# Kernel optimization log

Measured on AMD Instinct MI355X. Metric: run time of the kernel, lower is better.

## Reference

```python
import jax, jax.numpy as jnp
import numpy as np

N_NODES = 50000
N_EDGES = 800000
X_DIM = 32
S_DIM = 16
H_DIM = 96   # = 2 * (X_DIM + S_DIM), edge-MLP input
O_DIM = 64


def setup_inputs() -> dict:
    key = jax.random.key(0)
    ks = jax.random.split(key, 6)
    x = jax.random.normal(ks[0], (N_NODES, X_DIM), dtype=jnp.float32)
    scalars = jax.random.normal(ks[1], (1, S_DIM), dtype=jnp.float32)
    W1 = jax.random.normal(ks[2], (H_DIM, H_DIM), dtype=jnp.float32) * (1.0 / np.sqrt(H_DIM))
    b1 = jnp.zeros((H_DIM,), dtype=jnp.float32)
    W2 = jax.random.normal(ks[3], (H_DIM, O_DIM), dtype=jnp.float32) * (1.0 / np.sqrt(H_DIM))
    b2 = jnp.zeros((O_DIM,), dtype=jnp.float32)
    edge_index = jax.random.randint(ks[4], (2, N_EDGES), 0, N_NODES, dtype=jnp.int64)
    return {"x": x, "scalars": scalars, "W1": W1, "b1": b1, "W2": W2,
            "b2": b2, "edge_index": edge_index}


def reference(x, scalars, W1, b1, W2, b2, edge_index):
    n = x.shape[0]
    # single-graph branch of EFN: expand scalars to every node, concat
    s = jnp.broadcast_to(scalars.reshape(1, -1), (n, scalars.shape[-1]))
    h = jnp.concatenate([x, s], axis=1)                      # [N, 48]
    src, dst = edge_index[0], edge_index[1]
    # PTConv: edge-wise MLP on cat([x_i, x_j - x_i]), sum-aggregate to i (dst)
    h_i = h[dst]                                             # [E, 48] gather
    h_j = h[src]                                             # [E, 48] gather
    m_in = jnp.concatenate([h_i, h_j - h_i], axis=1)         # [E, 96]
    m = jax.nn.relu(m_in @ W1 + b1) @ W2 + b2                # [E, 64]
    out = jax.ops.segment_sum(m, dst, num_segments=n)        # [N, 64] scatter-add
    return out
```

## Files before the change

### kernel.cpp

```cpp
#include <hip/hip_runtime.h>


typedef _Float16 half8 __attribute__((ext_vector_type(8)));
typedef _Float16 half4 __attribute__((ext_vector_type(4)));
typedef _Float16 half2t __attribute__((ext_vector_type(2)));
typedef float f32x4 __attribute__((ext_vector_type(4)));
typedef float f32x2 __attribute__((ext_vector_type(2)));

#define LDK 72
#define LDW2 104
#define LDH 104
#define BCAP 1024
#define NBMAX 1563
#define BSTRIDE 16

static __device__ __forceinline__ unsigned char f32_to_fp8(float v) {
    int p = __builtin_amdgcn_cvt_pk_fp8_f32(v, v, 0, false);
    return (unsigned char)(p & 0xff);
}

__global__ __launch_bounds__(512) void prep_kernel(
    const float* __restrict__ x, const float* __restrict__ scalars,
    const float* __restrict__ W1, const float* __restrict__ b1,
    const float* __restrict__ W2, _Float16* __restrict__ W2T,
    _Float16* __restrict__ Pbuf, unsigned char* __restrict__ Qf8,
    const int* __restrict__ src, const int* __restrict__ dst,
    int* __restrict__ bcur, unsigned int* __restrict__ pairs,
    int tiles, int n_e4, int epb4, int nb, int nplace)
{
    __shared__ union {
        struct { int h[NBMAX]; int cur[NBMAX]; } pl;
        _Float16 sW[192 * LDK];
    } sm;
    const int tid = threadIdx.x;

    if ((int)blockIdx.x < nplace) {
        int* h = sm.pl.h;
        int* cur = sm.pl.cur;
        for (int b = tid; b < nb; b += 512) h[b] = 0;
        __syncthreads();

        const int base4 = blockIdx.x * epb4;
        for (int i = tid; i < epb4; i += 512) {
            int i4 = base4 + i;
            if (i4 < n_e4) {
                int4 d = ((const int4*)dst)[i4];
                atomicAdd(&h[d.x >> 5], 1);
                atomicAdd(&h[d.y >> 5], 1);
                atomicAdd(&h[d.z >> 5], 1);
                atomicAdd(&h[d.w >> 5], 1);
            }
        }
        __syncthreads();
        for (int b = tid; b < nb; b += 512) {
            int c = h[b];
            cur[b] = b * BCAP + (c ? atomicAdd(&bcur[b * BSTRIDE], c) : 0);
        }
        __syncthreads();
        for (int i = tid; i < epb4; i += 512) {
            int i4 = base4 + i;
            if (i4 < n_e4) {
                int4 s = ((const int4*)src)[i4];
                int4 d = ((const int4*)dst)[i4];
                int p;
                p = atomicAdd(&cur[d.x >> 5], 1);
                if (p < (d.x >> 5) * BCAP + BCAP) pairs[p] = (unsigned)s.x | ((unsigned)(d.x & 31) << 16);
                p = atomicAdd(&cur[d.y >> 5], 1);
                if (p < (d.y >> 5) * BCAP + BCAP) pairs[p] = (unsigned)s.y | ((unsigned)(d.y & 31) << 16);
                p = atomicAdd(&cur[d.z >> 5], 1);
                if (p < (d.z >> 5) * BCAP + BCAP) pairs[p] = (unsigned)s.z | ((unsigned)(d.z & 31) << 16);
                p = atomicAdd(&cur[d.w >> 5], 1);
                if (p < (d.w >> 5) * BCAP + BCAP) pairs[p] = (unsigned)s.w | ((unsigned)(d.w & 31) << 16);
            }
        }
    } else {
        _Float16* sW = sm.sW;
        for (int idx = tid; idx < 192 * 64; idx += 512) {
            int n = idx >> 6, k = idx & 63;
            float v = 0.f;
            if (k < 48)
                v = (n < 96) ? (W1[k * 96 + n] - W1[(k + 48) * 96 + n])
                             : W1[(k + 48) * 96 + (n - 96)];
            sW[n * LDK + k] = (_Float16)v;
        }
        const int pb = blockIdx.x - nplace;
        if (pb == 0) {
            for (int idx = tid; idx < 96 * 64; idx += 512) {
                int k = idx / 64, n = idx - k * 64;
                W2T[n * 96 + k] = (_Float16)W2[idx];
            }
        }
        __syncthreads();

        const int wave = tid >> 6, lane = tid & 63;
        const int quad = lane >> 4, r = lane & 15;
        const int stride = (gridDim.x - nplace) * 8;

        f32x4 bbv[6];
        #pragma unroll
        for (int nt = 0; nt < 6; ++nt)
            bbv[nt] = *(const f32x4*)&b1[nt * 16 + quad * 4];

        for (int tile = pb * 8 + wave; tile < tiles; tile += stride) {
            const int node = tile * 16 + r;

            half8 a0, a1;
            {
                const f32x4* xp = (const f32x4*)(x + (size_t)node * 32 + quad * 8);
                f32x4 v0 = xp[0], v1 = xp[1];
                #pragma unroll
                for (int j = 0; j < 4; ++j) {
                    a0[j] = (_Float16)v0[j];
                    a0[4 + j] = (_Float16)v1[j];
                }
                #pragma unroll
                for (int j = 0; j < 8; ++j) {
                    int k2 = 32 + quad * 8 + j;
                    a1[j] = (k2 < 48) ? (_Float16)scalars[k2 - 32] : (_Float16)0.f;
                }
            }

            #pragma unroll
            for (int nt = 0; nt < 12; ++nt) {
                f32x4 c = {0.f, 0.f, 0.f, 0.f};
                half8 b0 = *(const half8*)&sW[(nt * 16 + r) * LDK + quad * 8];
                half8 b1v = *(const half8*)&sW[(nt * 16 + r) * LDK + 32 + quad * 8];
                c = __builtin_amdgcn_mfma_f32_16x16x32_f16(b0, a0, c, 0, 0, 0);
                c = __builtin_amdgcn_mfma_f32_16x16x32_f16(b1v, a1, c, 0, 0, 0);
                if (nt < 6) {
                    const int colbase = nt * 16 + quad * 4;
                    half4 pv;
                    #pragma unroll
                    for (int i = 0; i < 4; ++i)
                        pv[i] = (_Float16)(c[i] + bbv[nt][i]);
                    *(half4*)&Pbuf[(size_t)node * 96 + colbase] = pv;
                } else {
                    const int colbase = (nt - 6) * 16 + quad * 4;
                    int lo = __builtin_amdgcn_cvt_pk_fp8_f32(c[0], c[1], 0, false);
                    int full = __builtin_amdgcn_cvt_pk_fp8_f32(c[2], c[3], lo, true);
                    *(unsigned int*)&Qf8[(size_t)node * 96 + colbase] = (unsigned)full;
                }
            }
        }
    }
}

static __device__ __forceinline__ void acc_edge(
    float* __restrict__ ac, const float* __restrict__ pf,
    unsigned int q0, unsigned int q1, unsigned int q2)
{
    f32x2 v;
    v = __builtin_amdgcn_cvt_pk_f32_fp8((int)q0, false);
    { float t0 = pf[0] + v[0], t1 = pf[1] + v[1];
      ac[0] += t0 > 0.f ? t0 : 0.f; ac[1] += t1 > 0.f ? t1 : 0.f; }
    v = __builtin_amdgcn_cvt_pk_f32_fp8((int)q0, true);
    { float t0 = pf[2] + v[0], t1 = pf[3] + v[1];
      ac[2] += t0 > 0.f ? t0 : 0.f; ac[3] += t1 > 0.f ? t1 : 0.f; }
    v = __builtin_amdgcn_cvt_pk_f32_fp8((int)q1, false);
    { float t0 = pf[4] + v[0], t1 = pf[5] + v[1];
      ac[4] += t0 > 0.f ? t0 : 0.f; ac[5] += t1 > 0.f ? t1 : 0.f; }
    v = __builtin_amdgcn_cvt_pk_f32_fp8((int)q1, true);
    { float t0 = pf[6] + v[0], t1 = pf[7] + v[1];
      ac[6] += t0 > 0.f ? t0 : 0.f; ac[7] += t1 > 0.f ? t1 : 0.f; }
    v = __builtin_amdgcn_cvt_pk_f32_fp8((int)q2, false);
    { float t0 = pf[8] + v[0], t1 = pf[9] + v[1];
      ac[8] += t0 > 0.f ? t0 : 0.f; ac[9] += t1 > 0.f ? t1 : 0.f; }
    v = __builtin_amdgcn_cvt_pk_f32_fp8((int)q2, true);
    { float t0 = pf[10] + v[0], t1 = pf[11] + v[1];
      ac[10] += t0 > 0.f ? t0 : 0.f; ac[11] += t1 > 0.f ? t1 : 0.f; }
}

__global__ __launch_bounds__(256) void sgo_kernel(
    const _Float16* __restrict__ Pbuf, const unsigned char* __restrict__ Qf8,
    const int* __restrict__ bcur, const unsigned int* __restrict__ pairs,
    const _Float16* __restrict__ W2T, const float* __restrict__ b2,
    float* __restrict__ out, int n_nodes)
{
    __shared__ unsigned short s_sorted[BCAP];
    __shared__ _Float16 sW2T[64 * LDW2];
    __shared__ _Float16 sH[32 * LDH];
    __shared__ int s_cnt[32];
    __shared__ int s_off[33];
    __shared__ int s_cur[32];

    const int b = blockIdx.x;
    const int tid = threadIdx.x;
    const int lo_g = b * BCAP;
    int cnt = bcur[b * BSTRIDE];
    if (cnt > BCAP) cnt = BCAP;

    half8 w2r[3];
    #pragma unroll
    for (int t = 0; t < 3; ++t) {
        int idx = tid + t * 256;
        int n = idx / 12, c = idx - n * 12;
        w2r[t] = *(const half8*)&W2T[n * 96 + c * 8];
    }

    const int wave = tid >> 6, lane = tid & 63;
    const int g = lane >> 3, j = lane & 7;
    const int ni = wave * 8 + g;
    const int node = b * 32 + ni;

    float pf[12];
    if (node < n_nodes) {
        const unsigned int* Pp = (const unsigned int*)(Pbuf + (size_t)node * 96);
        #pragma unroll
        for (int t = 0; t < 6; ++t) {
            half2t h = __builtin_bit_cast(half2t, Pp[j * 6 + t]);
            pf[2 * t] = (float)h[0];
            pf[2 * t + 1] = (float)h[1];
        }
    }

    unsigned int ureg[4];
    int nit = 0;
    for (int i = tid; i < cnt; i += 256) ureg[nit++] = pairs[lo_g + i];

    if (tid < 32) s_cnt[tid] = 0;
    __syncthreads();

    for (int t = 0; t < nit; ++t)
        atomicAdd(&s_cnt[(ureg[t] >> 16) & 31], 1);
    __syncthreads();
    if (tid == 0) {
        int a = 0;
        #pragma unroll
        for (int l = 0; l < 32; ++l) { s_off[l] = a; a += s_cnt[l]; }
        s_off[32] = a;
    }
    __syncthreads();
    if (tid < 32) s_cur[tid] = s_off[tid];
    __syncthreads();
    for (int t = 0; t < nit; ++t) {
        unsigned int u = ureg[t];
        int p = atomicAdd(&s_cur[(u >> 16) & 31], 1);
        s_sorted[p] = (unsigned short)(u & 0xffffu);
    }
    __syncthreads();

    #pragma unroll
    for (int t = 0; t < 3; ++t) {
        int idx = tid + t * 256;
        int n = idx / 12, c = idx - n * 12;
        *(half8*)&sW2T[n * LDW2 + c * 8] = w2r[t];
    }

    if (node < n_nodes) {
        const int lo = s_off[ni], hi = s_off[ni + 1];

        float ac[12];
        #pragma unroll
        for (int k = 0; k < 12; ++k) ac[k] = 0.f;

        if (lo < hi) {
            const int last = hi - 1;
            unsigned int A0, A1, A2, B0, B1, B2;
            {
                int s0 = s_sorted[lo];
                int i1 = lo + 1 <= last ? lo + 1 : last;
                int s1 = s_sorted[i1];
                const unsigned int* Q0 = (const unsigned int*)(Qf8 + (size_t)s0 * 96) + j * 3;
                const unsigned int* Q1 = (const unsigned int*)(Qf8 + (size_t)s1 * 96) + j * 3;
                A0 = Q0[0]; A1 = Q0[1]; A2 = Q0[2];
                B0 = Q1[0]; B1 = Q1[1]; B2 = Q1[2];
            }
            for (int i = lo; i < hi; i += 2) {
                int i2 = i + 2 <= last ? i + 2 : last;
                int i3 = i + 3 <= last ? i + 3 : last;
                int s2 = s_sorted[i2], s3 = s_sorted[i3];
                const unsigned int* Q2 = (const unsigned int*)(Qf8 + (size_t)s2 * 96) + j * 3;
                const unsigned int* Q3 = (const unsigned int*)(Qf8 + (size_t)s3 * 96) + j * 3;
                unsigned int NA0 = Q2[0], NA1 = Q2[1], NA2 = Q2[2];
                unsigned int NB0 = Q3[0], NB1 = Q3[1], NB2 = Q3[2];
                acc_edge(ac, pf, A0, A1, A2);
                if (i + 1 < hi) acc_edge(ac, pf, B0, B1, B2);
                A0 = NA0; A1 = NA1; A2 = NA2;
                B0 = NB0; B1 = NB1; B2 = NB2;
            }
        }

        unsigned int* Hp = (unsigned int*)sH + ni * (LDH / 2);
        #pragma unroll
        for (int t = 0; t < 6; ++t) {
            half2t hv;
            hv[0] = (_Float16)ac[2 * t];
            hv[1] = (_Float16)ac[2 * t + 1];
            Hp[j * 6 + t] = __builtin_bit_cast(unsigned int, hv);
        }
    }
    __syncthreads();

    const int quad = lane >> 4, r = lane & 15;
    const int t = wave >> 1;
    const int nt0 = (wave & 1) * 2;

    half8 a[3];
    #pragma unroll
    for (int kk = 0; kk < 3; ++kk)
        a[kk] = *(const half8*)&sH[(t * 16 + r) * LDH + kk * 32 + quad * 8];

    #pragma unroll
    for (int w = 0; w < 2; ++w) {
        const int nt = nt0 + w;
        f32x4 c = {0.f, 0.f, 0.f, 0.f};
        #pragma unroll
        for (int kk = 0; kk < 3; ++kk) {
            half8 bfrag = *(const half8*)&sW2T[(nt * 16 + r) * LDW2 + kk * 32 + quad * 8];
            c = __builtin_amdgcn_mfma_f32_16x16x32_f16(a[kk], bfrag, c, 0, 0, 0);
        }
        const int col = nt * 16 + r;
        const float bb = b2[col];
        #pragma unroll
        for (int i = 0; i < 4; ++i) {
            int local = t * 16 + quad * 4 + i;
            int nd = b * 32 + local;
            if (nd < n_nodes) {
                int dg = s_off[local + 1] - s_off[local];
                out[(size_t)nd * 64 + col] = c[i] + dg * bb;
            }
        }
    }
}

extern "C" void kernel_launch(void* const* d_in, const int* in_sizes, int n_in,
                              void* d_out, int out_size, void* d_ws, size_t ws_size,
                              hipStream_t stream) {
    const float* x       = (const float*)d_in[0];
    const float* scalars = (const float*)d_in[1];
    const float* W1      = (const float*)d_in[2];
    const float* b1      = (const float*)d_in[3];
    const float* W2      = (const float*)d_in[4];
    const float* b2      = (const float*)d_in[5];
    const int*   ei      = (const int*)d_in[6];
    float* out = (float*)d_out;

    const int n_edges = in_sizes[6] / 2;
    const int n_nodes = in_sizes[0] / 32;
    const int* src = ei;
    const int* dst = ei + n_edges;
    const int nb = (n_nodes + 31) / 32;
    const int tiles = n_nodes / 16;

    char* w = (char*)d_ws;
    _Float16* Pbuf = (_Float16*)w;          w += (size_t)n_nodes * 96 * 2;
    unsigned char* Qf8 = (unsigned char*)w; w += (size_t)n_nodes * 96;
    unsigned int* pairs = (unsigned int*)w; w += (size_t)nb * BCAP * 4;
    _Float16* W2T = (_Float16*)w;           w += (size_t)96 * 64 * 2;
    int* bcur = (int*)w;                    w += (size_t)nb * BSTRIDE * 4;

    hipMemsetAsync(bcur, 0, (size_t)nb * BSTRIDE * 4, stream);

    const int nplace = 80;
    const int n_e4 = n_edges / 4;
    const int epb4 = (n_e4 + nplace - 1) / nplace;
    prep_kernel<<<dim3(256), dim3(512), 0, stream>>>(
        x, scalars, W1, b1, W2, W2T, Pbuf, Qf8, src, dst, bcur, pairs,
        tiles, n_e4, epb4, nb, nplace);

    sgo_kernel<<<dim3(nb), dim3(256), 0, stream>>>(
        Pbuf, Qf8, bcur, pairs, W2T, b2, out, n_nodes);
}
```

Before: 122.0 us.

## Balance edge work across node groups with contiguous edge ranges and LDS atomics

Result: slower. 167.0 us (+36.9%).

```diff
diff --git a/kernel.cpp b/kernel.cpp
--- a/kernel.cpp
+++ b/kernel.cpp
@@ -9,7 +9,8 @@
 
 #define LDK 72
 #define LDW2 104
-#define LDH 104
+#define LDP 104
+#define LDHF 100
 #define BCAP 1024
 #define NBMAX 1563
 #define BSTRIDE 16
@@ -178,7 +179,8 @@
 {
     __shared__ unsigned short s_sorted[BCAP];
     __shared__ _Float16 sW2T[64 * LDW2];
-    __shared__ _Float16 sH[32 * LDH];
+    __shared__ float sHf[32 * LDHF];
+    __shared__ _Float16 sP[32 * LDP];
     __shared__ int s_cnt[32];
     __shared__ int s_off[33];
     __shared__ int s_cur[32];
@@ -189,29 +191,18 @@
     int cnt = bcur[b * BSTRIDE];
     if (cnt > BCAP) cnt = BCAP;
 
-    half8 w2r[3];
-    #pragma unroll
-    for (int t = 0; t < 3; ++t) {
-        int idx = tid + t * 256;
+    for (int idx = tid; idx < 768; idx += 256) {
         int n = idx / 12, c = idx - n * 12;
-        w2r[t] = *(const half8*)&W2T[n * 96 + c * 8];
-    }
-
-    const int wave = tid >> 6, lane = tid & 63;
-    const int g = lane >> 3, j = lane & 7;
-    const int ni = wave * 8 + g;
-    const int node = b * 32 + ni;
-
-    float pf[12];
-    if (node < n_nodes) {
-        const unsigned int* Pp = (const unsigned int*)(Pbuf + (size_t)node * 96);
-        #pragma unroll
-        for (int t = 0; t < 6; ++t) {
-            half2t h = __builtin_bit_cast(half2t, Pp[j * 6 + t]);
-            pf[2 * t] = (float)h[0];
-            pf[2 * t + 1] = (float)h[1];
-        }
-    }
+        *(half8*)&sW2T[n * LDW2 + c * 8] = *(const half8*)&W2T[n * 96 + c * 8];
+    }
+    for (int idx = tid; idx < 384; idx += 256) {
+        int n = idx / 12, c = idx - n * 12;
+        int nd = b * 32 + n;
+        half8 v = {};
+        if (nd < n_nodes) v = *(const half8*)&Pbuf[(size_t)nd * 96 + c * 8];
+        *(half8*)&sP[n * LDP + c * 8] = v;
+    }
+    for (int idx = tid; idx < 32 * LDHF; idx += 256) sHf[idx] = 0.f;
 
     unsigned int ureg[4];
     int nit = 0;
@@ -239,54 +230,79 @@
     }
     __syncthreads();
 
-    #pragma unroll
-    for (int t = 0; t < 3; ++t) {
-        int idx = tid + t * 256;
-        int n = idx / 12, c = idx - n * 12;
-        *(half8*)&sW2T[n * LDW2 + c * 8] = w2r[t];
-    }
-
-    if (node < n_nodes) {
-        const int lo = s_off[ni], hi = s_off[ni + 1];
-
-        float ac[12];
-        #pragma unroll
-        for (int k = 0; k < 12; ++k) ac[k] = 0.f;
+    const int wave = tid >> 6, lane = tid & 63;
+    const int g = lane >> 3, j = lane & 7;
+    const int gs = wave * 8 + g;
+
+    {
+        const int tot = s_off[32];
+        const int lo = (gs * tot) >> 5;
+        const int hi = ((gs + 1) * tot) >> 5;
 
         if (lo < hi) {
-            const int last = hi - 1;
-            unsigned int A0, A1, A2, B0, B1, B2;
+            int nc = 0;
+            #pragma unroll
+            for (int sh = 4; sh >= 0; --sh) {
+                int cand = nc + (1 << sh);
+                if (cand <= 31 && s_off[cand] <= lo) nc = cand;
+            }
+            int nend = s_off[nc + 1];
+
+            float pf[12];
+            {
+                const unsigned int* Pp = (const unsigned int*)&sP[nc * LDP];
+                #pragma unroll
+                for (int t = 0; t < 6; ++t) {
+                    half2t h = __builtin_bit_cast(half2t, Pp[j * 6 + t]);
+                    pf[2 * t] = (float)h[0];
+                    pf[2 * t + 1] = (float)h[1];
+                }
+            }
+
+            float ac[12];
+            #pragma unroll
+            for (int k = 0; k < 12; ++k) ac[k] = 0.f;
+            bool dirty = false;
+
+            unsigned int A0, A1, A2;
             {
                 int s0 = s_sorted[lo];
-                int i1 = lo + 1 <= last ? lo + 1 : last;
-                int s1 = s_sorted[i1];
-                const unsigned int* Q0 = (const unsigned int*)(Qf8 + (size_t)s0 * 96) + j * 3;
-                const unsigned int* Q1 = (const unsigned int*)(Qf8 + (size_t)s1 * 96) + j * 3;
-                A0 = Q0[0]; A1 = Q0[1]; A2 = Q0[2];
-                B0 = Q1[0]; B1 = Q1[1]; B2 = Q1[2];
-            }
-            for (int i = lo; i < hi; i += 2) {
-                int i2 = i + 2 <= last ? i + 2 : last;
-                int i3 = i + 3 <= last ? i + 3 : last;
-                int s2 = s_sorted[i2], s3 = s_sorted[i3];
-                const unsigned int* Q2 = (const unsigned int*)(Qf8 + (size_t)s2 * 96) + j * 3;
-                const unsigned int* Q3 = (const unsigned int*)(Qf8 + (size_t)s3 * 96) + j * 3;
-                unsigned int NA0 = Q2[0], NA1 = Q2[1], NA2 = Q2[2];
-                unsigned int NB0 = Q3[0], NB1 = Q3[1], NB2 = Q3[2];
-                acc_edge(ac, pf, A0, A1, A2);
-                if (i + 1 < hi) acc_edge(ac, pf, B0, B1, B2);
-                A0 = NA0; A1 = NA1; A2 = NA2;
-                B0 = NB0; B1 = NB1; B2 = NB2;
-            }
-        }
-
-        unsigned int* Hp = (unsigned int*)sH + ni * (LDH / 2);
-        #pragma unroll
-        for (int t = 0; t < 6; ++t) {
-            half2t hv;
-            hv[0] = (_Float16)ac[2 * t];
-            hv[1] = (_Float16)ac[2 * t + 1];
-            Hp[j * 6 + t] = __builtin_bit_cast(unsigned int, hv);
+                const unsigned int* Q = (const unsigned int*)(Qf8 + (size_t)s0 * 96) + j * 3;
+                A0 = Q[0]; A1 = Q[1]; A2 = Q[2];
+            }
+            for (int i = lo; i < hi; ++i) {
+                unsigned int N0 = 0, N1 = 0, N2 = 0;
+                if (i + 1 < hi) {
+                    int sn = s_sorted[i + 1];
+                    const unsigned int* Qn = (const unsigned int*)(Qf8 + (size_t)sn * 96) + j * 3;
+                    N0 = Qn[0]; N1 = Qn[1]; N2 = Qn[2];
+                }
+                while (i >= nend) {
+                    if (dirty) {
+                        #pragma unroll
+                        for (int k = 0; k < 12; ++k) {
+                            atomicAdd(&sHf[nc * LDHF + j * 12 + k], ac[k]);
+                            ac[k] = 0.f;
+                        }
+                        dirty = false;
+                    }
+                    ++nc; nend = s_off[nc + 1];
+                    const unsigned int* Pp = (const unsigned int*)&sP[nc * LDP];
+                    #pragma unroll
+                    for (int t = 0; t < 6; ++t) {
+                        half2t h = __builtin_bit_cast(half2t, Pp[j * 6 + t]);
+                        pf[2 * t] = (float)h[0];
+                        pf[2 * t + 1] = (float)h[1];
+                    }
+                }
+                acc_edge(ac, pf, A0, A1, A2); dirty = true;
+                A0 = N0; A1 = N1; A2 = N2;
+            }
+            if (dirty) {
+                #pragma unroll
+                for (int k = 0; k < 12; ++k)
+                    atomicAdd(&sHf[nc * LDHF + j * 12 + k], ac[k]);
+            }
         }
     }
     __syncthreads();
@@ -297,8 +313,18 @@
 
     half8 a[3];
     #pragma unroll
-    for (int kk = 0; kk < 3; ++kk)
-        a[kk] = *(const half8*)&sH[(t * 16 + r) * LDH + kk * 32 + quad * 8];
+    for (int kk = 0; kk < 3; ++kk) {
+        const float* hp = &sHf[(t * 16 + r) * LDHF + kk * 32 + quad * 8];
+        f32x4 v0 = *(const f32x4*)hp;
+        f32x4 v1 = *(const f32x4*)(hp + 4);
+        half8 av;
+        #pragma unroll
+        for (int e = 0; e < 4; ++e) {
+            av[e] = (_Float16)v0[e];
+            av[4 + e] = (_Float16)v1[e];
+        }
+        a[kk] = av;
+    }
 
     #pragma unroll
     for (int w = 0; w < 2; ++w) {
```
